# Kernel optimization log

Measured on AMD Instinct MI355X. Metric: run time of the kernel, lower is better.

## Reference

```python
import jax, jax.numpy as jnp
import numpy as np

B, C, IMG = 128, 3, 224
P = 16
NP = (IMG // P) ** 2          # 196 patches
S = 1 + NP                    # 197 tokens
D = 384
HEADS = 6
HD = D // HEADS               # 64
DEPTH = 12
HID = 4 * D                   # 1536
NCLS = 100
PATCH_DIM = C * P * P         # 768
EPS = 1e-5


def setup_inputs() -> dict:
    key = jax.random.key(0)
    ks = jax.random.split(key, 24)
    g = lambda k, shape, s=0.02: jax.random.normal(k, shape, dtype=jnp.float32) * s
    return {
        "x": jax.random.normal(ks[0], (B, C, IMG, IMG), dtype=jnp.float32),
        "patch_w": g(ks[1], (D, PATCH_DIM)),
        "patch_b": jnp.zeros((D,), jnp.float32),
        "cls_token": g(ks[2], (1, 1, D)),
        "pos_embed": g(ks[3], (1, S, D)),
        "ln1_g": jnp.ones((DEPTH, D), jnp.float32),
        "ln1_b": jnp.zeros((DEPTH, D), jnp.float32),
        "qkv_w": g(ks[4], (DEPTH, 3 * D, D)),
        "qkv_b": jnp.zeros((DEPTH, 3 * D), jnp.float32),
        "out_w": g(ks[5], (DEPTH, D, D)),
        "out_b": jnp.zeros((DEPTH, D), jnp.float32),
        "ln2_g": jnp.ones((DEPTH, D), jnp.float32),
        "ln2_b": jnp.zeros((DEPTH, D), jnp.float32),
        "fc1_w": g(ks[6], (DEPTH, HID, D)),
        "fc1_b": jnp.zeros((DEPTH, HID), jnp.float32),
        "fc2_w": g(ks[7], (DEPTH, D, HID)),
        "fc2_b": jnp.zeros((DEPTH, D), jnp.float32),
        "lnf_g": jnp.ones((D,), jnp.float32),
        "lnf_b": jnp.zeros((D,), jnp.float32),
        "head_w": g(ks[8], (NCLS, D)),
    }


def _ln(x, g, b):
    m = jnp.mean(x, axis=-1, keepdims=True)
    v = jnp.mean(jnp.square(x - m), axis=-1, keepdims=True)
    return (x - m) * jax.lax.rsqrt(v + EPS) * g + b


def reference(x, patch_w, patch_b, cls_token, pos_embed,
              ln1_g, ln1_b, qkv_w, qkv_b, out_w, out_b,
              ln2_g, ln2_b, fc1_w, fc1_b, fc2_w, fc2_b,
              lnf_g, lnf_b, head_w):
    b = x.shape[0]
    hp = IMG // P
    # patchify: unfold(2,P).unfold(3,P).permute(0,2,3,1,4,5) -> [B, N, C*P*P]
    patches = x.reshape(b, C, hp, P, hp, P).transpose(0, 2, 4, 1, 3, 5).reshape(b, NP, PATCH_DIM)
    tok = patches @ patch_w.T + patch_b                           # [B, NP, D]
    h = jnp.concatenate([jnp.broadcast_to(cls_token, (b, 1, D)), tok], axis=1)
    h = h + pos_embed[:, :S, :]
    scale = 1.0 / np.sqrt(HD).astype(np.float32)
    for i in range(DEPTH):
        xn = _ln(h, ln1_g[i], ln1_b[i])
        qkv = xn @ qkv_w[i].T + qkv_b[i]                          # [B, S, 3D]
        q, k, v = jnp.split(qkv, 3, axis=-1)
        q = q.reshape(b, S, HEADS, HD).transpose(0, 2, 1, 3) * scale
        k = k.reshape(b, S, HEADS, HD).transpose(0, 2, 1, 3)
        v = v.reshape(b, S, HEADS, HD).transpose(0, 2, 1, 3)
        attn = jax.nn.softmax(jnp.einsum('bhqd,bhkd->bhqk', q, k), axis=-1)
        ctx = jnp.einsum('bhqk,bhkd->bhqd', attn, v)
        ctx = ctx.transpose(0, 2, 1, 3).reshape(b, S, D)
        h = h + (ctx @ out_w[i].T + out_b[i])
        xn2 = _ln(h, ln2_g[i], ln2_b[i])
        hid = jax.nn.gelu(xn2 @ fc1_w[i].T + fc1_b[i], approximate=False)
        h = h + (hid @ fc2_w[i].T + fc2_b[i])
    cls = _ln(h[:, 0], lnf_g, lnf_b)
    return cls @ head_w.T                                         # [B, NCLS]
```

## Files before the change

### kernel.cpp

```cpp
#include <hip/hip_runtime.h>
#include <hip/hip_bf16.h>


#define S_ 197
#define D_ 384
#define BATCH 128

using bf16 = __hip_bfloat16;
typedef __attribute__((ext_vector_type(8))) __bf16 bf16x8;
typedef __attribute__((ext_vector_type(4))) float f32x4;

#if __has_builtin(__builtin_amdgcn_global_load_lds)
#define HAVE_GLL 1
__device__ __forceinline__ void gll16(const bf16* g, __bf16* l) {
  __builtin_amdgcn_global_load_lds(
      (const __attribute__((address_space(1))) void*)g,
      (__attribute__((address_space(3))) void*)l, 16, 0, 0);
}
#else
#define HAVE_GLL 0
#endif

__global__ __launch_bounds__(256) void k_f2b(const float* __restrict__ src,
                                             bf16* __restrict__ dst, int n4) {
  int i = blockIdx.x * 256 + threadIdx.x;
  if (i >= n4) return;
  float4 v = ((const float4*)src)[i];
  bf16 o[4] = {__float2bfloat16(v.x), __float2bfloat16(v.y),
               __float2bfloat16(v.z), __float2bfloat16(v.w)};
  ((uint2*)dst)[i] = *(uint2*)o;
}

__global__ __launch_bounds__(256) void k_embed_init(const float* __restrict__ cls,
                                                    const float* __restrict__ pos,
                                                    float* __restrict__ h) {
  int idx = blockIdx.x * 256 + threadIdx.x;
  if (idx >= BATCH * S_ * D_) return;
  int d = idx % D_;
  int s = (idx / D_) % S_;
  float v = pos[s * D_ + d];
  if (s == 0) v += cls[d];
  h[idx] = v;
}

__global__ __launch_bounds__(256) void k_patchify(const float* __restrict__ x,
                                                  bf16* __restrict__ patches) {
  int idx = blockIdx.x * 256 + threadIdx.x;
  if (idx >= BATCH * 196 * 768) return;
  int f = idx % 768;
  int n = (idx / 768) % 196;
  int b = idx / (768 * 196);
  int c = f >> 8, rem = f & 255, dy = rem >> 4, dx = rem & 15;
  int py = n / 14, px = n % 14;
  patches[idx] = __float2bfloat16(
      x[(((size_t)b * 3 + c) * 224 + py * 16 + dy) * 224 + px * 16 + dx]);
}

template <int MODE>
__global__ __launch_bounds__(512, 6) void k_gemm(const bf16* __restrict__ X,
                                                 const bf16* __restrict__ W,
                                                 const float* __restrict__ bias,
                                                 bf16* __restrict__ out,
                                                 float* __restrict__ res,
                                                 int N, int K, int remap) {
  __shared__ __align__(16) __bf16 As[2][128 * 32];
  __shared__ __align__(16) __bf16 Bs[2][128 * 32];
  const int tid = threadIdx.x;

  const int gx = gridDim.x;
  const int nwg = gx * gridDim.y;
  const int lid = blockIdx.y * gx + blockIdx.x;
  const int xcd = lid & 7, sseq = lid >> 3;
  const int q8 = nwg >> 3, r8 = nwg & 7;
  const int start = xcd * q8 + (xcd < r8 ? xcd : r8);
  const int wgid = start + sseq;
  const int m0 = (wgid / gx) * 128, n0 = (wgid % gx) * 128;

  const int lane = tid & 63, w = tid >> 6;
  const int wr = w >> 2, wc = w & 3;
  const int l16 = lane & 15, quad = lane >> 4;
  f32x4 acc[4][2] = {};

  const int srow = w * 16 + (lane >> 2);
  const int scol = (((lane & 3) ^ ((lane >> 3) & 3)) << 3);
  const bf16* Ag = X + (size_t)(m0 + srow) * K + scol;
  const bf16* Bg = W + (size_t)(n0 + srow) * K + scol;
  const int ldsW = w * 512;

  const int jx8 = ((quad ^ ((l16 >> 1) & 3)) << 3);
  const int aoff = (wr * 64 + l16) * 32 + jx8;
  const int boff = (wc * 32 + l16) * 32 + jx8;

#if HAVE_GLL
#define STAGE(buf, k0)                 \
  do {                                 \
    gll16(Ag + (k0), &As[buf][ldsW]);  \
    gll16(Bg + (k0), &Bs[buf][ldsW]);  \
  } while (0)
#else
#define STAGE(buf, k0)                                                \
  do {                                                                \
    *(uint4*)(&As[buf][ldsW + (lane >> 2) * 32 + (lane & 3) * 8]) =   \
        *(const uint4*)(Ag + (k0));                                   \
    *(uint4*)(&Bs[buf][ldsW + (lane >> 2) * 32 + (lane & 3) * 8]) =   \
        *(const uint4*)(Bg + (k0));                                   \
  } while (0)
#endif

  STAGE(0, 0);
  __syncthreads();
  for (int k0 = 0; k0 < K; k0 += 32) {
    const int cb = (k0 >> 5) & 1;
    if (k0 + 32 < K) STAGE(cb ^ 1, k0 + 32);
    bf16x8 av[4], bv[2];
#pragma unroll
    for (int i = 0; i < 4; i++)
      av[i] = *(const bf16x8*)(&As[cb][aoff + i * 512]);
#pragma unroll
    for (int j = 0; j < 2; j++)
      bv[j] = *(const bf16x8*)(&Bs[cb][boff + j * 512]);
#pragma unroll
    for (int i = 0; i < 4; i++)
#pragma unroll
      for (int j = 0; j < 2; j++)
        acc[i][j] = __builtin_amdgcn_mfma_f32_16x16x32_bf16(av[i], bv[j], acc[i][j], 0, 0, 0);
    __syncthreads();
  }
#undef STAGE

  float bvv[2];
#pragma unroll
  for (int j = 0; j < 2; j++)
    bvv[j] = bias[n0 + wc * 32 + j * 16 + l16];
#pragma unroll
  for (int i = 0; i < 4; i++) {
    const int rbase = m0 + wr * 64 + i * 16 + quad * 4;
#pragma unroll
    for (int j = 0; j < 2; j++) {
      const int col = n0 + wc * 32 + j * 16 + l16;
      const int which = col / 384;
      const int hd2 = (col >> 6) % 6;
      const int d = col & 63;
#pragma unroll
      for (int r = 0; r < 4; r++) {
        float v = acc[i][j][r] + bvv[j];
        int rw = rbase + r;
        if (MODE == 0) {
          out[(size_t)rw * N + col] = __float2bfloat16(v);
        } else if (MODE == 1) {
          float t = 0.7978845608f * v * (1.f + 0.044715f * v * v);
          float e = __expf(2.f * t);
          float th = 1.f - 2.f / (e + 1.f);
          out[(size_t)rw * N + col] = __float2bfloat16(0.5f * v * (1.f + th));
        } else if (MODE == 3) {
          int b2 = rw / 197;
          int s = rw - b2 * 197;
          out[((size_t)(which * 768 + b2 * 6 + hd2) * 197 + s) * 64 + d] =
              __float2bfloat16(v);
        } else {
          int hr = remap ? (rw + rw / 196 + 1) : rw;
          res[(size_t)hr * N + col] += v;
        }
      }
    }
  }
}

__global__ __launch_bounds__(128) void k_ln(const float* __restrict__ h,
                                            const float* __restrict__ g,
                                            const float* __restrict__ bt,
                                            bf16* __restrict__ xn) {
  const int r = blockIdx.x, t = threadIdx.x;
  const float* row = h + (size_t)r * D_;
  float x0 = row[t], x1 = row[t + 128], x2 = row[t + 256];
  float s = x0 + x1 + x2;
  float q = x0 * x0 + x1 * x1 + x2 * x2;
#pragma unroll
  for (int o = 32; o; o >>= 1) {
    s += __shfl_xor(s, o);
    q += __shfl_xor(q, o);
  }
  __shared__ float rs[2], rq[2];
  if ((t & 63) == 0) { rs[t >> 6] = s; rq[t >> 6] = q; }
  __syncthreads();
  s = rs[0] + rs[1];
  q = rq[0] + rq[1];
  const float mean = s * (1.f / 384.f);
  const float var = q * (1.f / 384.f) - mean * mean;
  const float rstd = rsqrtf(var + 1e-5f);
  bf16* o = xn + (size_t)r * D_;
  o[t] = __float2bfloat16((x0 - mean) * rstd * g[t] + bt[t]);
  o[t + 128] = __float2bfloat16((x1 - mean) * rstd * g[t + 128] + bt[t + 128]);
  o[t + 256] = __float2bfloat16((x2 - mean) * rstd * g[t + 256] + bt[t + 256]);
}

__global__ __launch_bounds__(256) void k_attn(const bf16* __restrict__ qkv,
                                              bf16* __restrict__ ctx) {
  const int bh = blockIdx.x;
  const int b = bh / 6, hd = bh % 6;
  const bf16* Qg = qkv + (size_t)bh * 12608;
  const bf16* Kg = qkv + (size_t)(768 + bh) * 12608;
  const bf16* Vg = qkv + (size_t)(1536 + bh) * 12608;
  __shared__ __align__(16) __bf16 Vt[64 * 232];
  __shared__ __align__(16) __bf16 Ps[4][16 * 232];
  const int tid = threadIdx.x;
  const int lane = tid & 63, w = tid >> 6;
  const int l16 = lane & 15, quad = lane >> 4;
  const __bf16 z = (__bf16)0.0f;

  for (int i = tid; i < 64 * 35; i += 256) {
    int d = i / 35, k = 197 + i % 35;
    Vt[d * 232 + k] = z;
  }
  for (int i = tid; i < S_ * 64; i += 256) {
    int k = i >> 6, d = i & 63;
    Vt[d * 232 + k] = *(const __bf16*)&Vg[(size_t)k * 64 + d];
  }
  for (int i = lane; i < 16 * 24; i += 64) {
    int r = i / 24, c = 208 + i % 24;
    Ps[w][r * 232 + c] = z;
  }
  __syncthreads();

  const bf16x8 zf = {};
  for (int band = w; band < 13; band += 4) {
    const int qrow = band * 16 + l16;
    bf16x8 aq0 = zf, aq1 = zf;
    if (qrow < S_) {
      aq0 = *(const bf16x8*)(Qg + (size_t)qrow * 64 + quad * 8);
      aq1 = *(const bf16x8*)(Qg + (size_t)qrow * 64 + 32 + quad * 8);
    }
    f32x4 sc[13];
#pragma unroll
    for (int t = 0; t < 13; t++) {
      const int krow = t * 16 + l16;
      bf16x8 bk0 = zf, bk1 = zf;
      if (krow < S_) {
        bk0 = *(const bf16x8*)(Kg + (size_t)krow * 64 + quad * 8);
        bk1 = *(const bf16x8*)(Kg + (size_t)krow * 64 + 32 + quad * 8);
      }
      f32x4 a = {};
      a = __builtin_amdgcn_mfma_f32_16x16x32_bf16(aq0, bk0, a, 0, 0, 0);
      a = __builtin_amdgcn_mfma_f32_16x16x32_bf16(aq1, bk1, a, 0, 0, 0);
      sc[t] = a;
    }
#pragma unroll
    for (int t = 0; t < 13; t++)
#pragma unroll
      for (int r = 0; r < 4; r++) sc[t][r] *= 0.125f;
    if (l16 >= 5) {
#pragma unroll
      for (int r = 0; r < 4; r++) sc[12][r] = -1e30f;
    }
    f32x4 mx = sc[0];
#pragma unroll
    for (int t = 1; t < 13; t++)
#pragma unroll
      for (int r = 0; r < 4; r++) mx[r] = fmaxf(mx[r], sc[t][r]);
#pragma unroll
    for (int o = 1; o < 16; o <<= 1)
#pragma unroll
      for (int r = 0; r < 4; r++) mx[r] = fmaxf(mx[r], __shfl_xor(mx[r], o));
    f32x4 sum = {};
#pragma unroll
    for (int t = 0; t < 13; t++)
#pragma unroll
      for (int r = 0; r < 4; r++) {
        float p = __expf(sc[t][r] - mx[r]);
        sc[t][r] = p;
        sum[r] += p;
      }
#pragma unroll
    for (int o = 1; o < 16; o <<= 1)
#pragma unroll
      for (int r = 0; r < 4; r++) sum[r] += __shfl_xor(sum[r], o);
    f32x4 rinv;
#pragma unroll
    for (int r = 0; r < 4; r++) rinv[r] = 1.0f / sum[r];
#pragma unroll
    for (int t = 0; t < 13; t++)
#pragma unroll
      for (int r = 0; r < 4; r++)
        Ps[w][(quad * 4 + r) * 232 + t * 16 + l16] = (__bf16)sc[t][r];
    f32x4 oacc[4] = {};
#pragma unroll
    for (int ks = 0; ks < 7; ks++) {
      bf16x8 pa = *(const bf16x8*)&Ps[w][l16 * 232 + ks * 32 + quad * 8];
#pragma unroll
      for (int c = 0; c < 4; c++) {
        bf16x8 bv = *(const bf16x8*)&Vt[(c * 16 + l16) * 232 + ks * 32 + quad * 8];
        oacc[c] = __builtin_amdgcn_mfma_f32_16x16x32_bf16(pa, bv, oacc[c], 0, 0, 0);
      }
    }
    const int orow = band * 16 + quad * 4;
#pragma unroll
    for (int c = 0; c < 4; c++)
#pragma unroll
      for (int r = 0; r < 4; r++) {
        const int rw = orow + r;
        if (rw < S_)
          ctx[((size_t)b * S_ + rw) * D_ + hd * 64 + c * 16 + l16] =
              __float2bfloat16(oacc[c][r] * rinv[r]);
      }
  }
}

__global__ __launch_bounds__(128) void k_head(const float* __restrict__ h,
                                              const float* __restrict__ g,
                                              const float* __restrict__ bt,
                                              const float* __restrict__ hw,
                                              float* __restrict__ out) {
  const int b = blockIdx.x, t = threadIdx.x;
  const float* row = h + (size_t)b * S_ * D_;
  float x0 = row[t], x1 = row[t + 128], x2 = row[t + 256];
  float s = x0 + x1 + x2;
  float q = x0 * x0 + x1 * x1 + x2 * x2;
#pragma unroll
  for (int o = 32; o; o >>= 1) {
    s += __shfl_xor(s, o);
    q += __shfl_xor(q, o);
  }
  __shared__ float rs[2], rq[2];
  if ((t & 63) == 0) { rs[t >> 6] = s; rq[t >> 6] = q; }
  __syncthreads();
  s = rs[0] + rs[1];
  q = rq[0] + rq[1];
  const float mean = s * (1.f / 384.f);
  const float var = q * (1.f / 384.f) - mean * mean;
  const float rstd = rsqrtf(var + 1e-5f);
  __shared__ float clsn[384];
  clsn[t] = (x0 - mean) * rstd * g[t] + bt[t];
  clsn[t + 128] = (x1 - mean) * rstd * g[t + 128] + bt[t + 128];
  clsn[t + 256] = (x2 - mean) * rstd * g[t + 256] + bt[t + 256];
  __syncthreads();
  if (t < 100) {
    const float* wr = hw + (size_t)t * D_;
    float a = 0.f;
    for (int d = 0; d < 384; d++) a += clsn[d] * wr[d];
    out[b * 100 + t] = a;
  }
}

extern "C" void kernel_launch(void* const* d_in, const int* in_sizes, int n_in,
                              void* d_out, int out_size, void* d_ws, size_t ws_size,
                              hipStream_t stream) {
  (void)in_sizes; (void)n_in; (void)out_size; (void)ws_size;
  const float* x       = (const float*)d_in[0];
  const float* patch_w = (const float*)d_in[1];
  const float* patch_b = (const float*)d_in[2];
  const float* cls_tok = (const float*)d_in[3];
  const float* pos_emb = (const float*)d_in[4];
  const float* ln1_g   = (const float*)d_in[5];
  const float* ln1_b   = (const float*)d_in[6];
  const float* qkv_w   = (const float*)d_in[7];
  const float* qkv_b   = (const float*)d_in[8];
  const float* out_w   = (const float*)d_in[9];
  const float* out_b   = (const float*)d_in[10];
  const float* ln2_g   = (const float*)d_in[11];
  const float* ln2_b   = (const float*)d_in[12];
  const float* fc1_w   = (const float*)d_in[13];
  const float* fc1_b   = (const float*)d_in[14];
  const float* fc2_w   = (const float*)d_in[15];
  const float* fc2_b   = (const float*)d_in[16];
  const float* lnf_g   = (const float*)d_in[17];
  const float* lnf_b   = (const float*)d_in[18];
  const float* head_w  = (const float*)d_in[19];
  float* out = (float*)d_out;

  const size_t R = (size_t)BATCH * S_;
  char* p = (char*)d_ws;
  float* h  = (float*)p; p += R * 384 * 4;
  bf16* xn  = (bf16*)p;  p += R * 384 * 2;
  bf16* u   = (bf16*)p;  p += R * 1536 * 2;
  bf16* qkvb = u;
  bf16* ctxb = u + R * 1152;
  bf16* hidb = u;
  bf16* patches = u;
  bf16* wb  = (bf16*)p;
  bf16* patch_wb = wb;
  bf16* qkv_wb   = patch_wb + 294912;
  bf16* out_wb   = qkv_wb + 5308416;
  bf16* fc1_wb   = out_wb + 1769472;
  bf16* fc2_wb   = fc1_wb + 7077888;

  k_f2b<<<dim3((294912 / 4 + 255) / 256), dim3(256), 0, stream>>>(patch_w, patch_wb, 294912 / 4);
  k_f2b<<<dim3((5308416 / 4 + 255) / 256), dim3(256), 0, stream>>>(qkv_w, qkv_wb, 5308416 / 4);
  k_f2b<<<dim3((1769472 / 4 + 255) / 256), dim3(256), 0, stream>>>(out_w, out_wb, 1769472 / 4);
  k_f2b<<<dim3((7077888 / 4 + 255) / 256), dim3(256), 0, stream>>>(fc1_w, fc1_wb, 7077888 / 4);
  k_f2b<<<dim3((7077888 / 4 + 255) / 256), dim3(256), 0, stream>>>(fc2_w, fc2_wb, 7077888 / 4);

  k_embed_init<<<dim3((BATCH * S_ * D_) / 256), dim3(256), 0, stream>>>(cls_tok, pos_emb, h);
  k_patchify<<<dim3((BATCH * 196 * 768) / 256), dim3(256), 0, stream>>>(x, patches);
  k_gemm<2><<<dim3(3, 196), dim3(512), 0, stream>>>(patches, patch_wb, patch_b, nullptr, h, 384, 768, 1);

  for (int i = 0; i < 12; i++) {
    k_ln<<<dim3((unsigned)R), dim3(128), 0, stream>>>(h, ln1_g + i * 384, ln1_b + i * 384, xn);
    k_gemm<3><<<dim3(9, 197), dim3(512), 0, stream>>>(xn, qkv_wb + (size_t)i * 1152 * 384,
                                                      qkv_b + i * 1152, qkvb, nullptr, 1152, 384, 0);
    k_attn<<<dim3(768), dim3(256), 0, stream>>>(qkvb, ctxb);
    k_gemm<2><<<dim3(3, 197), dim3(512), 0, stream>>>(ctxb, out_wb + (size_t)i * 384 * 384,
                                                      out_b + i * 384, nullptr, h, 384, 384, 0);
    k_ln<<<dim3((unsigned)R), dim3(128), 0, stream>>>(h, ln2_g + i * 384, ln2_b + i * 384, xn);
    k_gemm<1><<<dim3(12, 197), dim3(512), 0, stream>>>(xn, fc1_wb + (size_t)i * 1536 * 384,
                                                       fc1_b + i * 1536, hidb, nullptr, 1536, 384, 0);
    k_gemm<2><<<dim3(3, 197), dim3(512), 0, stream>>>(hidb, fc2_wb + (size_t)i * 384 * 1536,
                                                      fc2_b + i * 384, nullptr, h, 384, 1536, 0);
  }
  k_head<<<dim3(128), dim3(128), 0, stream>>>(h, lnf_g, lnf_b, head_w, out);
}
```

Before: 3.228 ms.

## Fuse residual-add GEMMs with following LayerNorm via full-row tiles

Adds a GEMM kernel where each block computes a 32-row by full 384-column tile, so after adding bias and residual into h it can compute row mean/variance in-block and write the normalized bf16 activations for the next GEMM. This replaces the out-proj and fc2 GEMMs plus both per-layer LayerNorm launches, removing 24 LN kernel launches and their re-read of h. The trade-off is a narrower M tile with a large B tile in LDS, which may cut occupancy or GEMM efficiency compared with the old 2D-tiled kernel. Variance is computed as E[x^2]-mean^2 rather than the two-pass form.

```diff
diff --git a/kernel.cpp b/kernel.cpp
--- a/kernel.cpp
+++ b/kernel.cpp
@@ -164,6 +164,144 @@
       }
     }
   }
+}
+
+__global__ __launch_bounds__(256, 4) void k_gemm_ln(
+    const bf16* __restrict__ X, const bf16* __restrict__ W,
+    const float* __restrict__ bias, float* __restrict__ res,
+    bf16* __restrict__ xn, const float* __restrict__ lng,
+    const float* __restrict__ lnb, int K) {
+  __shared__ __align__(16) __bf16 As[2][32 * 32];
+  __shared__ __align__(16) __bf16 Bs[2][384 * 32];
+  __shared__ float ps[32][4], qs[32][4];
+  const int tid = threadIdx.x;
+  const int m0 = blockIdx.x * 32;
+  const int lane = tid & 63, w = tid >> 6;
+  const int wc = w;
+  const int l16 = lane & 15, quad = lane >> 4;
+  f32x4 acc[2][6] = {};
+
+  const int scol = (((lane & 3) ^ ((lane >> 3) & 3)) << 3);
+  const bf16* Ag = X + (size_t)(m0 + w * 16 + (lane >> 2)) * K + scol;
+  const bf16* Bg = W + (size_t)(w * 16 + (lane >> 2)) * K + scol;
+
+  const int jx8 = ((quad ^ ((l16 >> 1) & 3)) << 3);
+  const int aoff = l16 * 32 + jx8;
+  const int boff = (wc * 96 + l16) * 32 + jx8;
+
+#if HAVE_GLL
+#define STAGEL(buf, k0)                                                   \
+  do {                                                                    \
+    if (w < 2) gll16(Ag + (k0), &As[buf][w * 512]);                       \
+    _Pragma("unroll") for (int o = 0; o < 6; o++)                         \
+        gll16(Bg + (size_t)o * 64 * K + (k0),                             \
+              &Bs[buf][(o * 64 + w * 16) * 32]);                          \
+  } while (0)
+#else
+#define STAGEL(buf, k0)                                                   \
+  do {                                                                    \
+    if (w < 2)                                                            \
+      *(uint4*)(&As[buf][(w * 16 + (lane >> 2)) * 32 + (lane & 3) * 8]) = \
+          *(const uint4*)(Ag + (k0));                                     \
+    _Pragma("unroll") for (int o = 0; o < 6; o++)                         \
+        *(uint4*)(&Bs[buf][(o * 64 + w * 16 + (lane >> 2)) * 32 +         \
+                           (lane & 3) * 8]) =                             \
+            *(const uint4*)(Bg + (size_t)o * 64 * K + (k0));              \
+  } while (0)
+#endif
+
+  STAGEL(0, 0);
+  __syncthreads();
+  for (int k0 = 0; k0 < K; k0 += 32) {
+    const int cb = (k0 >> 5) & 1;
+    if (k0 + 32 < K) STAGEL(cb ^ 1, k0 + 32);
+    bf16x8 av[2], bv[6];
+#pragma unroll
+    for (int i = 0; i < 2; i++)
+      av[i] = *(const bf16x8*)(&As[cb][aoff + i * 512]);
+#pragma unroll
+    for (int j = 0; j < 6; j++)
+      bv[j] = *(const bf16x8*)(&Bs[cb][boff + j * 512]);
+#pragma unroll
+    for (int i = 0; i < 2; i++)
+#pragma unroll
+      for (int j = 0; j < 6; j++)
+        acc[i][j] = __builtin_amdgcn_mfma_f32_16x16x32_bf16(av[i], bv[j], acc[i][j], 0, 0, 0);
+    __syncthreads();
+  }
+#undef STAGEL
+
+  float bb[6];
+#pragma unroll
+  for (int j = 0; j < 6; j++) bb[j] = bias[wc * 96 + j * 16 + l16];
+#pragma unroll
+  for (int i = 0; i < 2; i++)
+#pragma unroll
+    for (int r = 0; r < 4; r++) {
+      const int hr = m0 + i * 16 + quad * 4 + r;
+#pragma unroll
+      for (int j = 0; j < 6; j++) {
+        const int col = wc * 96 + j * 16 + l16;
+        float nv = res[(size_t)hr * 384 + col] + acc[i][j][r] + bb[j];
+        res[(size_t)hr * 384 + col] = nv;
+        acc[i][j][r] = nv;
+      }
+    }
+  float s_[2][4], q_[2][4];
+#pragma unroll
+  for (int i = 0; i < 2; i++)
+#pragma unroll
+    for (int r = 0; r < 4; r++) {
+      float s = 0.f, q = 0.f;
+#pragma unroll
+      for (int j = 0; j < 6; j++) {
+        float v = acc[i][j][r];
+        s += v;
+        q += v * v;
+      }
+#pragma unroll
+      for (int o = 1; o < 16; o <<= 1) {
+        s += __shfl_xor(s, o);
+        q += __shfl_xor(q, o);
+      }
+      s_[i][r] = s;
+      q_[i][r] = q;
+    }
+  if (l16 == 0) {
+#pragma unroll
+    for (int i = 0; i < 2; i++)
+#pragma unroll
+      for (int r = 0; r < 4; r++) {
+        const int lr = i * 16 + quad * 4 + r;
+        ps[lr][w] = s_[i][r];
+        qs[lr][w] = q_[i][r];
+      }
+  }
+  __syncthreads();
+  float gg[6], bt[6];
+#pragma unroll
+  for (int j = 0; j < 6; j++) {
+    gg[j] = lng[wc * 96 + j * 16 + l16];
+    bt[j] = lnb[wc * 96 + j * 16 + l16];
+  }
+#pragma unroll
+  for (int i = 0; i < 2; i++)
+#pragma unroll
+    for (int r = 0; r < 4; r++) {
+      const int lr = i * 16 + quad * 4 + r;
+      const float s = ps[lr][0] + ps[lr][1] + ps[lr][2] + ps[lr][3];
+      const float q = qs[lr][0] + qs[lr][1] + qs[lr][2] + qs[lr][3];
+      const float mean = s * (1.f / 384.f);
+      const float var = q * (1.f / 384.f) - mean * mean;
+      const float rstd = rsqrtf(var + 1e-5f);
+      const int hr = m0 + lr;
+#pragma unroll
+      for (int j = 0; j < 6; j++) {
+        const int col = wc * 96 + j * 16 + l16;
+        xn[(size_t)hr * 384 + col] =
+            __float2bfloat16((acc[i][j][r] - mean) * rstd * gg[j] + bt[j]);
+      }
+    }
 }
 
 __global__ __launch_bounds__(128) void k_ln(const float* __restrict__ h,
@@ -393,18 +531,21 @@
   k_patchify<<<dim3((BATCH * 196 * 768) / 256), dim3(256), 0, stream>>>(x, patches);
   k_gemm<2><<<dim3(3, 196), dim3(512), 0, stream>>>(patches, patch_wb, patch_b, nullptr, h, 384, 768, 1);
 
+  k_ln<<<dim3((unsigned)R), dim3(128), 0, stream>>>(h, ln1_g, ln1_b, xn);
+
   for (int i = 0; i < 12; i++) {
-    k_ln<<<dim3((unsigned)R), dim3(128), 0, stream>>>(h, ln1_g + i * 384, ln1_b + i * 384, xn);
     k_gemm<3><<<dim3(9, 197), dim3(512), 0, stream>>>(xn, qkv_wb + (size_t)i * 1152 * 384,
                                                       qkv_b + i * 1152, qkvb, nullptr, 1152, 384, 0);
     k_attn<<<dim3(768), dim3(256), 0, stream>>>(qkvb, ctxb);
-    k_gemm<2><<<dim3(3, 197), dim3(512), 0, stream>>>(ctxb, out_wb + (size_t)i * 384 * 384,
-                                                      out_b + i * 384, nullptr, h, 384, 384, 0);
-    k_ln<<<dim3((unsigned)R), dim3(128), 0, stream>>>(h, ln2_g + i * 384, ln2_b + i * 384, xn);
+    k_gemm_ln<<<dim3(788), dim3(256), 0, stream>>>(ctxb, out_wb + (size_t)i * 384 * 384,
+                                                   out_b + i * 384, h, xn,
+                                                   ln2_g + i * 384, ln2_b + i * 384, 384);
     k_gemm<1><<<dim3(12, 197), dim3(512), 0, stream>>>(xn, fc1_wb + (size_t)i * 1536 * 384,
                                                        fc1_b + i * 1536, hidb, nullptr, 1536, 384, 0);
-    k_gemm<2><<<dim3(3, 197), dim3(512), 0, stream>>>(hidb, fc2_wb + (size_t)i * 384 * 1536,
-                                                      fc2_b + i * 384, nullptr, h, 384, 1536, 0);
+    const int nx = (i + 1) % 12;
+    k_gemm_ln<<<dim3(788), dim3(256), 0, stream>>>(hidb, fc2_wb + (size_t)i * 384 * 1536,
+                                                   fc2_b + i * 384, h, xn,
+                                                   ln1_g + nx * 384, ln1_b + nx * 384, 1536);
   }
   k_head<<<dim3(128), dim3(128), 0, stream>>>(h, lnf_g, lnf_b, head_w, out);
 }
```

After: 3.745 ms. 1.16x slower.
